# Kernel optimization log

Measured on AMD Instinct MI355X. Metric: run time of the kernel, lower is better.

Reference implementation:

```python
import jax, jax.numpy as jnp
import numpy as np
from jax import lax

EPS = 1e-5
# PyTorch bicubic (a=-0.75), scale_factor=2, align_corners=False -> fixed 4-tap
# weights: even outputs use frac 0.75, odd outputs use frac 0.25.
W75 = jnp.array([-0.03515625, 0.26171875, 0.87890625, -0.10546875], dtype=jnp.float32)
W25 = W75[::-1]


def _up1d_2x(x, axis):
    x = jnp.moveaxis(x, axis, -1)
    n = x.shape[-1]
    pad = [(0, 0)] * (x.ndim - 1) + [(2, 2)]
    xp = jnp.pad(x, pad, mode='edge')  # replicate border like torch
    even = sum(W75[k] * xp[..., k:k + n] for k in range(4))
    odd = sum(W25[k] * xp[..., k + 1:k + 1 + n] for k in range(4))
    out = jnp.stack([even, odd], axis=-1).reshape(x.shape[:-1] + (2 * n,))
    return jnp.moveaxis(out, -1, axis)


def bicubic2x(x):  # [N,C,H,W] -> [N,C,2H,2W]
    return _up1d_2x(_up1d_2x(x, 2), 3)


def groupnorm1(x, w, b):  # GroupNorm(1, C): normalize over (C,H,W) per sample
    m = jnp.mean(x, axis=(1, 2, 3), keepdims=True)
    v = jnp.mean(jnp.square(x - m), axis=(1, 2, 3), keepdims=True)
    xh = (x - m) * lax.rsqrt(v + EPS)
    return xh * w[None, :, None, None] + b[None, :, None, None]


def conv3x3(x, w, b):
    y = lax.conv_general_dilated(x, w, (1, 1), ((1, 1), (1, 1)),
                                 dimension_numbers=('NCHW', 'OIHW', 'NCHW'))
    return y + b[None, :, None, None]


def setup_inputs() -> dict:
    key = jax.random.key(0)
    ks = jax.random.split(key, 24)
    B, C, H, W = 4, 256, 64, 64
    chans = [256, 64, 16, 4]  # embed_dim // 4**i
    inp = {'x': jax.random.normal(ks[0], (B, C, H, W), jnp.float32)}
    for j in range(4):
        s = 2 ** (j + 1)
        inp[f'em{j}'] = 0.1 * jax.random.normal(ks[1 + j], (B, chans[j], H * s, W * s), jnp.float32)
    for j, c in enumerate(chans):
        co = max(c // 4, 1)
        inp[f'gn_w{j}'] = 1.0 + 0.1 * jax.random.normal(ks[5 + 4 * j], (c,), jnp.float32)
        inp[f'gn_b{j}'] = 0.1 * jax.random.normal(ks[6 + 4 * j], (c,), jnp.float32)
        inp[f'cw{j}'] = jax.random.normal(ks[7 + 4 * j], (co, c, 3, 3), jnp.float32) / np.sqrt(9.0 * c)
        inp[f'cb{j}'] = 0.01 * jax.random.normal(ks[8 + 4 * j], (co,), jnp.float32)
    # per-sample (left, top, right, bottom) in the 64x64 grid; host-side ints
    # (in the original these come from get_bbox_from_mask on CPU)
    inp['bboxes'] = np.array([[8, 4, 56, 60], [0, 0, 48, 40],
                              [16, 8, 64, 56], [4, 12, 40, 64]], dtype=np.int32)
    return inp


def reference(x, em0, em1, em2, em3,
              gn_w0, gn_b0, cw0, cb0, gn_w1, gn_b1, cw1, cb1,
              gn_w2, gn_b2, cw2, cb2, gn_w3, gn_b3, cw3, cb3, bboxes):
    ems = [em0, em1, em2, em3]
    gws = [gn_w0, gn_w1, gn_w2, gn_w3]
    gbs = [gn_b0, gn_b1, gn_b2, gn_b3]
    cws = [cw0, cw1, cw2, cw3]
    cbs = [cb0, cb1, cb2, cb3]
    bb = np.asarray(bboxes)
    strides = [2, 4, 8, 16]
    B, _, H, W = x.shape
    mask = jnp.full((B, 1, H * 16, W * 16), -100.0, dtype=x.dtype)
    for i in range(B):  # per-sample ragged regions, as in the original eval loop
        l, t, r, b = (int(v) for v in bb[i])
        z = x[i:i + 1, :, t:b, l:r]
        for j in range(4):
            z = groupnorm1(z, gws[j], gbs[j])
            z = bicubic2x(z)
            s = strides[j]
            z = z + ems[j][i:i + 1, :, t * s:b * s, l * s:r * s]
            z = conv3x3(z, cws[j], cbs[j])
            if j < 3:
                z = jax.nn.silu(z)
        s = strides[-1]
        mask = mask.at[i:i + 1, :, t * s:b * s, l * s:r * s].set(z)
    return mask
```

## Files before the change

### kernel.cpp

```cpp
#include <hip/hip_runtime.h>

#define EPS 1e-5f

__global__ void fill_kernel(float* __restrict__ out, int n, float v) {
    int i = blockIdx.x * blockDim.x + threadIdx.x;
    if (i < n) out[i] = v;
}

__global__ void zero8_kernel(float* __restrict__ a) {
    if (threadIdx.x < 8) a[threadIdx.x] = 0.f;
}

__global__ void gn_reduce_kernel(const float* __restrict__ in, long long inBatchStride,
                                 int inPitch, long long inPlane, int useOrig,
                                 int c, int shift, const int* __restrict__ bboxes,
                                 int batch0, float* __restrict__ accs)
{
    int batch = batch0 + blockIdx.z;
    const int* bb = bboxes + 4 * batch;
    int l = bb[0], t = bb[1], r = bb[2], btm = bb[3];
    int h = (btm - t) << shift;
    int w = (r   - l) << shift;
    int oy = useOrig ? t : 0;
    int ox = useOrig ? l : 0;
    const float* base = in + (long long)blockIdx.z * inBatchStride;

    float s = 0.f, s2 = 0.f;
    int stride = gridDim.x * blockDim.x;

    if (((w | ox | inPitch) & 3) == 0) {
        int w4 = w >> 2;
        int count4 = c * h * w4;
        for (int idx = blockIdx.x * blockDim.x + threadIdx.x; idx < count4; idx += stride) {
            int xw   = idx % w4;
            int rest = idx / w4;
            int y    = rest % h;
            int ch   = rest / h;
            const float4 v = *reinterpret_cast<const float4*>(
                base + (long long)ch * inPlane + (long long)(y + oy) * inPitch + (ox + 4 * xw));
            s  += (v.x + v.y) + (v.z + v.w);
            s2 += (v.x * v.x + v.y * v.y) + (v.z * v.z + v.w * v.w);
        }
    } else {
        int count = c * h * w;
        for (int idx = blockIdx.x * blockDim.x + threadIdx.x; idx < count; idx += stride) {
            int xw   = idx % w;
            int rest = idx / w;
            int y    = rest % h;
            int ch   = rest / h;
            float v = base[(long long)ch * inPlane + (long long)(y + oy) * inPitch + (xw + ox)];
            s  += v;
            s2 += v * v;
        }
    }

    for (int off = 32; off > 0; off >>= 1) {
        s  += __shfl_down(s, off);
        s2 += __shfl_down(s2, off);
    }
    __shared__ float red[2][4];
    int wid = threadIdx.x >> 6;
    if ((threadIdx.x & 63) == 0) { red[0][wid] = s; red[1][wid] = s2; }
    __syncthreads();
    if (threadIdx.x == 0) {
        float ts = (red[0][0] + red[0][1]) + (red[0][2] + red[0][3]);
        float t2 = (red[1][0] + red[1][1]) + (red[1][2] + red[1][3]);
        atomicAdd(&accs[2 * batch],     ts);
        atomicAdd(&accs[2 * batch + 1], t2);
    }
}

__global__ void normup_kernel(const float* __restrict__ in, long long inBatchStride,
                              int inPitch, long long inPlane, int useOrig,
                              const float* __restrict__ em, long long emBatchStride, int emPitch,
                              const float* __restrict__ gw, const float* __restrict__ gb,
                              const float* __restrict__ accs,
                              float* __restrict__ outB, long long outBatchStride, int outPitch,
                              int c, int shift, const int* __restrict__ bboxes,
                              int batch0, int tilesY)
{
    int batch = batch0 + blockIdx.z;
    const int* bb = bboxes + 4 * batch;
    int l = bb[0], t = bb[1], r = bb[2], btm = bb[3];
    int h = (btm - t) << shift;
    int w = (r   - l) << shift;
    int H2 = 2 * h, W2 = 2 * w;

    int ch = blockIdx.y / tilesY;
    int ty = blockIdx.y % tilesY;
    int y2 = ty * 16 + threadIdx.y;
    int x2 = blockIdx.x * 16 + threadIdx.x;
    if (y2 >= H2 || x2 >= W2) return;

    float count = (float)(c * h * w);
    float m  = accs[2 * batch] / count;
    float var = accs[2 * batch + 1] / count - m * m;
    float rs = rsqrtf(fmaxf(var, 0.f) + EPS);
    float alpha = rs * gw[ch];
    float beta  = gb[ch] - m * alpha;

    int oy = useOrig ? t : 0;
    int ox = useOrig ? l : 0;
    const float* base = in + (long long)blockIdx.z * inBatchStride + (long long)ch * inPlane;

    const float Wv[2][4] = {
        {-0.03515625f, 0.26171875f, 0.87890625f, -0.10546875f},
        {-0.10546875f, 0.87890625f, 0.26171875f, -0.03515625f}};

    int iy = y2 >> 1, py = y2 & 1;
    int ix = x2 >> 1, px = x2 & 1;
    int by = iy - 2 + py;
    int bx = ix - 2 + px;

    float acc = 0.f;
    #pragma unroll
    for (int a = 0; a < 4; a++) {
        int ry = by + a;
        ry = ry < 0 ? 0 : (ry > h - 1 ? h - 1 : ry);
        const float* rowp = base + (long long)(ry + oy) * inPitch + ox;
        float rsum = 0.f;
        #pragma unroll
        for (int q = 0; q < 4; q++) {
            int rx = bx + q;
            rx = rx < 0 ? 0 : (rx > w - 1 ? w - 1 : rx);
            rsum += Wv[px][q] * rowp[rx];
        }
        acc += Wv[py][a] * rsum;
    }

    float val = alpha * acc + beta;
    int S = 2 << shift;
    val += em[(long long)blockIdx.z * emBatchStride + (long long)ch * emPitch * emPitch
              + (long long)(t * S + y2) * emPitch + (l * S + x2)];

    outB[(long long)blockIdx.z * outBatchStride + (long long)ch * outPitch * outPitch
         + (long long)y2 * outPitch + x2] = val;
}

#define CICH 4

template<int COT>
__global__ void __launch_bounds__(256)
conv_reg_kernel(const float* __restrict__ inB, long long inBatchStride, int inPitch,
                const float* __restrict__ wts, const float* __restrict__ bias,
                int cin, int doSilu,
                float* __restrict__ out, long long outBatchStride, int outPitch,
                int toMask, int shift, const int* __restrict__ bboxes,
                int batch0, int tilesY)
{
    int batch = batch0 + blockIdx.z;
    const int* bb = bboxes + 4 * batch;
    int l = bb[0], t = bb[1], r = bb[2], btm = bb[3];
    int h = (btm - t) << shift;
    int w = (r   - l) << shift;
    int H2 = 2 * h, W2 = 2 * w;

    int og = blockIdx.y / tilesY;
    int ty = blockIdx.y % tilesY;
    int oc0 = og * COT;
    int y0 = ty * 32;
    int x0 = blockIdx.x * 32;
    if (y0 >= H2 || x0 >= W2) return;

    int ly = threadIdx.y, lx = threadIdx.x;
    int tid = ly * 16 + lx;
    int py0 = y0 + 2 * ly;
    int px0 = x0 + 2 * lx;

    __shared__ float tile[CICH][34][36];
    __shared__ __align__(16) float wsh[COT][CICH][12];

    const float* base = inB + (long long)blockIdx.z * inBatchStride;
    long long plane = (long long)inPitch * inPitch;

    float acc[COT][2][2];
    #pragma unroll
    for (int o = 0; o < COT; o++)
        #pragma unroll
        for (int rr = 0; rr < 2; rr++)
            #pragma unroll
            for (int ss = 0; ss < 2; ss++) acc[o][rr][ss] = 0.f;

    for (int ci0 = 0; ci0 < cin; ci0 += CICH) {
        for (int q = tid; q < CICH * 1156; q += 256) {
            int p   = q / 1156;
            int rem = q - p * 1156;
            int yy  = rem / 34;
            int xx  = rem - yy * 34;
            int gy = y0 - 1 + yy, gx = x0 - 1 + xx;
            float v = (gy >= 0 && gy < H2 && gx >= 0 && gx < W2)
                          ? base[(long long)(ci0 + p) * plane + (long long)gy * inPitch + gx]
                          : 0.f;
            tile[p][yy][xx] = v;
        }
        for (int q = tid; q < COT * CICH * 9; q += 256) {
            int o   = q / (CICH * 9);
            int rem = q - o * (CICH * 9);
            int p   = rem / 9;
            int k   = rem - p * 9;
            wsh[o][p][k] = wts[((long long)(oc0 + o) * cin + (ci0 + p)) * 9 + k];
        }
        __syncthreads();

        #pragma unroll
        for (int p = 0; p < CICH; p++) {
            float v[4][4];
            #pragma unroll
            for (int rr = 0; rr < 4; rr++) {
                const float2 a = *reinterpret_cast<const float2*>(&tile[p][2 * ly + rr][2 * lx]);
                const float2 b = *reinterpret_cast<const float2*>(&tile[p][2 * ly + rr][2 * lx + 2]);
                v[rr][0] = a.x; v[rr][1] = a.y; v[rr][2] = b.x; v[rr][3] = b.y;
            }
            #pragma unroll
            for (int o = 0; o < COT; o++) {
                const float4 wA = *reinterpret_cast<const float4*>(&wsh[o][p][0]);
                const float4 wB = *reinterpret_cast<const float4*>(&wsh[o][p][4]);
                const float  w8 = wsh[o][p][8];
                #pragma unroll
                for (int rr = 0; rr < 2; rr++) {
                    #pragma unroll
                    for (int ss = 0; ss < 2; ss++) {
                        acc[o][rr][ss] += wA.x * v[rr    ][ss] + wA.y * v[rr    ][ss + 1] + wA.z * v[rr    ][ss + 2]
                                        + wA.w * v[rr + 1][ss] + wB.x * v[rr + 1][ss + 1] + wB.y * v[rr + 1][ss + 2]
                                        + wB.z * v[rr + 2][ss] + wB.w * v[rr + 2][ss + 1] + w8   * v[rr + 2][ss + 2];
                    }
                }
            }
        }
        __syncthreads();
    }

    #pragma unroll
    for (int o = 0; o < COT; o++) {
        float b = bias[oc0 + o];
        #pragma unroll
        for (int rr = 0; rr < 2; rr++) {
            #pragma unroll
            for (int ss = 0; ss < 2; ss++) {
                int oy2 = py0 + rr, ox2 = px0 + ss;
                if (oy2 >= H2 || ox2 >= W2) continue;
                float v = acc[o][rr][ss] + b;
                if (doSilu) v = v / (1.f + __expf(-v));
                if (toMask) {
                    int S = 2 << shift;
                    out[(long long)batch * 1024 * 1024 + (long long)(t * S + oy2) * 1024 + (l * S + ox2)] = v;
                } else {
                    out[(long long)blockIdx.z * outBatchStride + (long long)(oc0 + o) * outPitch * outPitch
                        + (long long)oy2 * outPitch + ox2] = v;
                }
            }
        }
    }
}

static inline void launch_conv(int co, int tiles32, int nz, const float* inB, long long inBS, int inPitch,
                               const float* wts, const float* bias, int cin, int doSilu,
                               float* out, long long outBS, int outPitch,
                               int toMask, int shift, const int* bboxes, int batch0,
                               hipStream_t stream)
{
    dim3 blk(16, 16);
    if (co == 64) {
        conv_reg_kernel<8><<<dim3(tiles32, tiles32 * 8, nz), blk, 0, stream>>>(
            inB, inBS, inPitch, wts, bias, cin, doSilu, out, outBS, outPitch,
            toMask, shift, bboxes, batch0, tiles32);
    } else if (co == 16) {
        conv_reg_kernel<8><<<dim3(tiles32, tiles32 * 2, nz), blk, 0, stream>>>(
            inB, inBS, inPitch, wts, bias, cin, doSilu, out, outBS, outPitch,
            toMask, shift, bboxes, batch0, tiles32);
    } else if (co == 4) {
        conv_reg_kernel<4><<<dim3(tiles32, tiles32, nz), blk, 0, stream>>>(
            inB, inBS, inPitch, wts, bias, cin, doSilu, out, outBS, outPitch,
            toMask, shift, bboxes, batch0, tiles32);
    } else {
        conv_reg_kernel<1><<<dim3(tiles32, tiles32, nz), blk, 0, stream>>>(
            inB, inBS, inPitch, wts, bias, cin, doSilu, out, outBS, outPitch,
            toMask, shift, bboxes, batch0, tiles32);
    }
}

extern "C" void kernel_launch(void* const* d_in, const int* in_sizes, int n_in,
                              void* d_out, int out_size, void* d_ws, size_t ws_size,
                              hipStream_t stream)
{
    const float* x  = (const float*)d_in[0];
    const float* em[4];
    const float* gw[4];
    const float* gb[4];
    const float* cw[4];
    const float* cb[4];
    for (int j = 0; j < 4; j++) {
        em[j] = (const float*)d_in[1 + j];
        gw[j] = (const float*)d_in[5 + 4 * j];
        gb[j] = (const float*)d_in[6 + 4 * j];
        cw[j] = (const float*)d_in[7 + 4 * j];
        cb[j] = (const float*)d_in[8 + 4 * j];
    }
    const int* bboxes = (const int*)d_in[21];
    float* out = (float*)d_out;
    float* ws  = (float*)d_ws;

    const int chans[4] = {256, 64, 16, 4};
    const int couts[4] = {64, 16, 4, 1};

    const long long A_OFF  = 256;
    const long long A_SLOT = 1048576;
    const long long B_SLOT = 4194304;

    bool par = ws_size >= (size_t)(A_OFF + 4 * A_SLOT + 4 * B_SLOT) * 4;
    int nA = par ? 4 : 1;
    float* accs = ws;
    float* bufA = ws + A_OFF;
    float* bufB = ws + A_OFF + nA * A_SLOT;

    fill_kernel<<<(4194304 + 255) / 256, 256, 0, stream>>>(out, 4194304, -100.0f);

    if (par) {
        for (int j = 0; j < 4; j++) {
            int c = chans[j], co = couts[j], shift = j;
            int inPitch = 64 << j;
            long long inPlane = (long long)inPitch * inPitch;
            int upPitch = 128 << j;
            int tiles = upPitch / 16;
            int tiles32 = upPitch / 32;
            int E = 128 << j;
            long long emStride = (long long)c * E * E;

            const float* gin = (j == 0) ? x : bufA;
            long long ginStride = (j == 0) ? (long long)256 * 64 * 64 : A_SLOT;
            int useOrig = (j == 0) ? 1 : 0;

            zero8_kernel<<<1, 64, 0, stream>>>(accs);
            gn_reduce_kernel<<<dim3(512, 1, 4), 256, 0, stream>>>(
                gin, ginStride, inPitch, inPlane, useOrig, c, shift, bboxes, 0, accs);
            normup_kernel<<<dim3(tiles, tiles * c, 4), dim3(16, 16), 0, stream>>>(
                gin, ginStride, inPitch, inPlane, useOrig,
                em[j], emStride, E, gw[j], gb[j], accs,
                bufB, B_SLOT, upPitch, c, shift, bboxes, 0, tiles);
            launch_conv(co, tiles32, 4,
                        bufB, B_SLOT, upPitch, cw[j], cb[j], c, (j < 3) ? 1 : 0,
                        (j < 3) ? bufA : out, (j < 3) ? A_SLOT : 0, upPitch,
                        (j == 3) ? 1 : 0, shift, bboxes, 0, stream);
        }
    } else {
        for (int i = 0; i < 4; i++) {
            for (int j = 0; j < 4; j++) {
                int c = chans[j], co = couts[j], shift = j;
                int inPitch = 64 << j;
                long long inPlane = (long long)inPitch * inPitch;
                int upPitch = 128 << j;
                int tiles = upPitch / 16;
                int tiles32 = upPitch / 32;
                int E = 128 << j;
                long long emStride = (long long)c * E * E;

                const float* gin = (j == 0) ? (x + (long long)i * 256 * 64 * 64) : bufA;
                int useOrig = (j == 0) ? 1 : 0;

                zero8_kernel<<<1, 64, 0, stream>>>(accs);
                gn_reduce_kernel<<<dim3(512, 1, 1), 256, 0, stream>>>(
                    gin, 0, inPitch, inPlane, useOrig, c, shift, bboxes, i, accs);
                normup_kernel<<<dim3(tiles, tiles * c, 1), dim3(16, 16), 0, stream>>>(
                    gin, 0, inPitch, inPlane, useOrig,
                    em[j] + (long long)i * emStride, 0, E, gw[j], gb[j], accs,
                    bufB, 0, upPitch, c, shift, bboxes, i, tiles);
                launch_conv(co, tiles32, 1,
                            bufB, 0, upPitch, cw[j], cb[j], c, (j < 3) ? 1 : 0,
                            (j < 3) ? bufA : out, 0, upPitch,
                            (j == 3) ? 1 : 0, shift, bboxes, i, stream);
            }
        }
    }
}
```

Measured before the change: 1.755 ms.

## Split conv input channels across blocks with atomic accumulation for early stages

The first two conv stages now split their input-channel reduction four ways across extra grid z-slices, and each slice accumulates partial sums into the output with atomicAdd. A zero-fill kernel runs before the conv and a finalize kernel runs after it to add the bias and apply SiLU. The aim is to raise block count and occupancy for these low-parallelism, high-cin convolutions. In exchange it adds two full-buffer passes, atomic traffic, and a non-deterministic summation order.

```diff
diff --git a/kernel.cpp b/kernel.cpp
--- a/kernel.cpp
+++ b/kernel.cpp
@@ -9,6 +9,19 @@
 
 __global__ void zero8_kernel(float* __restrict__ a) {
     if (threadIdx.x < 8) a[threadIdx.x] = 0.f;
+}
+
+__global__ void finalize_kernel(float* __restrict__ buf, long long batchStride,
+                                int n, int ocShift, const float* __restrict__ bias,
+                                int doSilu)
+{
+    int idx = blockIdx.x * blockDim.x + threadIdx.x;
+    if (idx >= n) return;
+    float* p = buf + (long long)blockIdx.y * batchStride;
+    int oc = idx >> ocShift;
+    float v = p[idx] + bias[oc];
+    if (doSilu) v = v / (1.f + __expf(-v));
+    p[idx] = v;
 }
 
 __global__ void gn_reduce_kernel(const float* __restrict__ in, long long inBatchStride,
@@ -143,12 +156,14 @@
 __global__ void __launch_bounds__(256)
 conv_reg_kernel(const float* __restrict__ inB, long long inBatchStride, int inPitch,
                 const float* __restrict__ wts, const float* __restrict__ bias,
-                int cin, int doSilu,
+                int cin, int ciPer, int bShift, int doSilu,
                 float* __restrict__ out, long long outBatchStride, int outPitch,
-                int toMask, int shift, const int* __restrict__ bboxes,
+                int toMask, int doFinal, int shift, const int* __restrict__ bboxes,
                 int batch0, int tilesY)
 {
-    int batch = batch0 + blockIdx.z;
+    int zb = blockIdx.z & ((1 << bShift) - 1);
+    int sp = blockIdx.z >> bShift;
+    int batch = batch0 + zb;
     const int* bb = bboxes + 4 * batch;
     int l = bb[0], t = bb[1], r = bb[2], btm = bb[3];
     int h = (btm - t) << shift;
@@ -170,8 +185,9 @@
     __shared__ float tile[CICH][34][36];
     __shared__ __align__(16) float wsh[COT][CICH][12];
 
-    const float* base = inB + (long long)blockIdx.z * inBatchStride;
+    const float* base = inB + (long long)zb * inBatchStride;
     long long plane = (long long)inPitch * inPitch;
+    long long oplane = (long long)outPitch * outPitch;
 
     float acc[COT][2][2];
     #pragma unroll
@@ -181,7 +197,9 @@
             #pragma unroll
             for (int ss = 0; ss < 2; ss++) acc[o][rr][ss] = 0.f;
 
-    for (int ci0 = 0; ci0 < cin; ci0 += CICH) {
+    int ciStart = sp * ciPer;
+    int ciEnd = ciStart + ciPer;
+    for (int ci0 = ciStart; ci0 < ciEnd; ci0 += CICH) {
         for (int q = tid; q < CICH * 1156; q += 256) {
             int p   = q / 1156;
             int rem = q - p * 1156;
@@ -230,52 +248,73 @@
         __syncthreads();
     }
 
-    #pragma unroll
-    for (int o = 0; o < COT; o++) {
-        float b = bias[oc0 + o];
+    if (doFinal) {
         #pragma unroll
-        for (int rr = 0; rr < 2; rr++) {
+        for (int o = 0; o < COT; o++) {
+            float b = bias[oc0 + o];
             #pragma unroll
-            for (int ss = 0; ss < 2; ss++) {
-                int oy2 = py0 + rr, ox2 = px0 + ss;
-                if (oy2 >= H2 || ox2 >= W2) continue;
-                float v = acc[o][rr][ss] + b;
-                if (doSilu) v = v / (1.f + __expf(-v));
-                if (toMask) {
-                    int S = 2 << shift;
-                    out[(long long)batch * 1024 * 1024 + (long long)(t * S + oy2) * 1024 + (l * S + ox2)] = v;
-                } else {
-                    out[(long long)blockIdx.z * outBatchStride + (long long)(oc0 + o) * outPitch * outPitch
-                        + (long long)oy2 * outPitch + ox2] = v;
+            for (int rr = 0; rr < 2; rr++) {
+                #pragma unroll
+                for (int ss = 0; ss < 2; ss++) {
+                    int oy2 = py0 + rr, ox2 = px0 + ss;
+                    if (oy2 >= H2 || ox2 >= W2) continue;
+                    float v = acc[o][rr][ss] + b;
+                    if (doSilu) v = v / (1.f + __expf(-v));
+                    if (toMask) {
+                        int S = 2 << shift;
+                        out[(long long)batch * 1024 * 1024 + (long long)(t * S + oy2) * 1024 + (l * S + ox2)] = v;
+                    } else {
+                        out[(long long)zb * outBatchStride + (long long)(oc0 + o) * oplane
+                            + (long long)oy2 * outPitch + ox2] = v;
+                    }
                 }
             }
         }
-    }
-}
-
-static inline void launch_conv(int co, int tiles32, int nz, const float* inB, long long inBS, int inPitch,
+    } else {
+        #pragma unroll
+        for (int o = 0; o < COT; o++) {
+            #pragma unroll
+            for (int rr = 0; rr < 2; rr++) {
+                #pragma unroll
+                for (int ss = 0; ss < 2; ss++) {
+                    int oy2 = py0 + rr, ox2 = px0 + ss;
+                    if (oy2 >= H2 || ox2 >= W2) continue;
+                    atomicAdd(&out[(long long)zb * outBatchStride + (long long)(oc0 + o) * oplane
+                                   + (long long)oy2 * outPitch + ox2], acc[o][rr][ss]);
+                }
+            }
+        }
+    }
+}
+
+static inline void launch_conv(int co, int tiles32, int nz, int S,
+                               const float* inB, long long inBS, int inPitch,
                                const float* wts, const float* bias, int cin, int doSilu,
                                float* out, long long outBS, int outPitch,
                                int toMask, int shift, const int* bboxes, int batch0,
                                hipStream_t stream)
 {
     dim3 blk(16, 16);
-    if (co == 64) {
-        conv_reg_kernel<8><<<dim3(tiles32, tiles32 * 8, nz), blk, 0, stream>>>(
-            inB, inBS, inPitch, wts, bias, cin, doSilu, out, outBS, outPitch,
-            toMask, shift, bboxes, batch0, tiles32);
-    } else if (co == 16) {
-        conv_reg_kernel<8><<<dim3(tiles32, tiles32 * 2, nz), blk, 0, stream>>>(
-            inB, inBS, inPitch, wts, bias, cin, doSilu, out, outBS, outPitch,
-            toMask, shift, bboxes, batch0, tiles32);
+    int bShift = (nz == 4) ? 2 : 0;
+    int ciPer = cin / S;
+    int doFinal = (S == 1) ? 1 : 0;
+    dim3 grid;
+    if (co == 64)      grid = dim3(tiles32, tiles32 * 8, nz * S);
+    else if (co == 16) grid = dim3(tiles32, tiles32 * 2, nz * S);
+    else               grid = dim3(tiles32, tiles32,     nz * S);
+
+    if (co == 64 || co == 16) {
+        conv_reg_kernel<8><<<grid, blk, 0, stream>>>(
+            inB, inBS, inPitch, wts, bias, cin, ciPer, bShift, doSilu,
+            out, outBS, outPitch, toMask, doFinal, shift, bboxes, batch0, tiles32);
     } else if (co == 4) {
-        conv_reg_kernel<4><<<dim3(tiles32, tiles32, nz), blk, 0, stream>>>(
-            inB, inBS, inPitch, wts, bias, cin, doSilu, out, outBS, outPitch,
-            toMask, shift, bboxes, batch0, tiles32);
+        conv_reg_kernel<4><<<grid, blk, 0, stream>>>(
+            inB, inBS, inPitch, wts, bias, cin, ciPer, bShift, doSilu,
+            out, outBS, outPitch, toMask, doFinal, shift, bboxes, batch0, tiles32);
     } else {
-        conv_reg_kernel<1><<<dim3(tiles32, tiles32, nz), blk, 0, stream>>>(
-            inB, inBS, inPitch, wts, bias, cin, doSilu, out, outBS, outPitch,
-            toMask, shift, bboxes, batch0, tiles32);
+        conv_reg_kernel<1><<<grid, blk, 0, stream>>>(
+            inB, inBS, inPitch, wts, bias, cin, ciPer, bShift, doSilu,
+            out, outBS, outPitch, toMask, doFinal, shift, bboxes, batch0, tiles32);
     }
 }
 
@@ -302,6 +341,7 @@
 
     const int chans[4] = {256, 64, 16, 4};
     const int couts[4] = {64, 16, 4, 1};
+    const int splits[4] = {4, 4, 1, 1};
 
     const long long A_OFF  = 256;
     const long long A_SLOT = 1048576;
@@ -325,6 +365,7 @@
             int tiles32 = upPitch / 32;
             int E = 128 << j;
             long long emStride = (long long)c * E * E;
+            int S = splits[j];
 
             const float* gin = (j == 0) ? x : bufA;
             long long ginStride = (j == 0) ? (long long)256 * 64 * 64 : A_SLOT;
@@ -337,10 +378,19 @@
                 gin, ginStride, inPitch, inPlane, useOrig,
                 em[j], emStride, E, gw[j], gb[j], accs,
                 bufB, B_SLOT, upPitch, c, shift, bboxes, 0, tiles);
-            launch_conv(co, tiles32, 4,
+            if (S > 1) {
+                fill_kernel<<<(int)((4 * A_SLOT + 255) / 256), 256, 0, stream>>>(
+                    bufA, (int)(4 * A_SLOT), 0.f);
+            }
+            launch_conv(co, tiles32, 4, S,
                         bufB, B_SLOT, upPitch, cw[j], cb[j], c, (j < 3) ? 1 : 0,
                         (j < 3) ? bufA : out, (j < 3) ? A_SLOT : 0, upPitch,
                         (j == 3) ? 1 : 0, shift, bboxes, 0, stream);
+            if (S > 1) {
+                int ocShift = 2 * (7 + j);
+                finalize_kernel<<<dim3(4096, 4), 256, 0, stream>>>(
+                    bufA, A_SLOT, (int)A_SLOT, ocShift, cb[j], (j < 3) ? 1 : 0);
+            }
         }
     } else {
         for (int i = 0; i < 4; i++) {
@@ -353,6 +403,7 @@
                 int tiles32 = upPitch / 32;
                 int E = 128 << j;
                 long long emStride = (long long)c * E * E;
+                int S = splits[j];
 
                 const float* gin = (j == 0) ? (x + (long long)i * 256 * 64 * 64) : bufA;
                 int useOrig = (j == 0) ? 1 : 0;
@@ -364,11 +415,20 @@
                     gin, 0, inPitch, inPlane, useOrig,
                     em[j] + (long long)i * emStride, 0, E, gw[j], gb[j], accs,
                     bufB, 0, upPitch, c, shift, bboxes, i, tiles);
-                launch_conv(co, tiles32, 1,
+                if (S > 1) {
+                    fill_kernel<<<(int)((A_SLOT + 255) / 256), 256, 0, stream>>>(
+                        bufA, (int)A_SLOT, 0.f);
+                }
+                launch_conv(co, tiles32, 1, S,
                             bufB, 0, upPitch, cw[j], cb[j], c, (j < 3) ? 1 : 0,
                             (j < 3) ? bufA : out, 0, upPitch,
                             (j == 3) ? 1 : 0, shift, bboxes, i, stream);
-            }
-        }
-    }
-}
+                if (S > 1) {
+                    int ocShift = 2 * (7 + j);
+                    finalize_kernel<<<dim3(4096, 1), 256, 0, stream>>>(
+                        bufA, 0, (int)A_SLOT, ocShift, cb[j], (j < 3) ? 1 : 0);
+                }
+            }
+        }
+    }
+}
```

New measurement: 1.797 ms. 2.4% more time.
